# Kernel tuning notes

Measured on AMD Instinct MI355X. Metric: run time of the kernel, lower is better.

The kernel has to match this reference:

```python
import jax, jax.numpy as jnp
import numpy as np


def _l2norm(t, eps=1e-12):
    # matches torch F.normalize(p=2, dim=-1): x / max(||x||_2, eps)
    n = jnp.sqrt(jnp.sum(t * t, axis=-1, keepdims=True))
    return t / jnp.maximum(n, eps)


def setup_inputs() -> dict:
    key = jax.random.key(0)
    ks = jax.random.split(key, 8)
    B, N, C, H, W = 16, 4, 256, 64, 64
    d = 64  # dim_head
    x = jax.random.normal(ks[0], (B, C, H, W), jnp.float32)
    fmaps = jax.random.normal(ks[1], (B, N, C, H, W), jnp.float32)
    Wq = jax.random.normal(ks[2], (N * d, C), jnp.float32) * 0.02   # Linear [out,in]
    Wk = jax.random.normal(ks[3], (N, d, C), jnp.float32) * 0.02    # grouped 1x1 conv, per-group [d,C]
    Wv = jax.random.normal(ks[4], (N, d, C), jnp.float32) * 0.02
    rescale = jnp.ones((N, 1, 1), jnp.float32)
    Wffn = jax.random.normal(ks[5], (C, N * d), jnp.float32) * 0.02
    bffn = jnp.zeros((C,), jnp.float32)
    return {"x": x, "fmaps": fmaps, "Wq": Wq, "Wk": Wk, "Wv": Wv,
            "rescale": rescale, "Wffn": Wffn, "bffn": bffn}


def reference(x, fmaps, Wq, Wk, Wv, rescale, Wffn, bffn):
    B, N, C, H, W = fmaps.shape
    d = Wk.shape[1]
    HW = H * W

    # x: [B,C,H,W] -> tokens [B,HW,C]
    x_in = jnp.transpose(x, (0, 2, 3, 1)).reshape(B, HW, C)
    q_in = jnp.einsum('bsc,oc->bso', x_in, Wq)            # [B,HW,N*d]

    # grouped 1x1 convs on fmaps (group = fmap index n)
    fm = fmaps.reshape(B, N, C, HW)                       # [B,N,C,HW]
    k = jnp.einsum('bncs,ndc->bnds', fm, Wk)              # [B,N,d,HW]
    v = jnp.einsum('bncs,ndc->bnds', fm, Wv)              # [B,N,d,HW]

    q = jnp.transpose(q_in.reshape(B, HW, N, d), (0, 2, 3, 1))  # [B,N,d,HW]

    qn = _l2norm(q)   # normalize over spatial (HW) axis
    kn = _l2norm(k)

    attn = jnp.einsum('bnds,bnes->bnde', kn, qn) * rescale      # [B,N,d,d]
    attn = jax.nn.softmax(attn, axis=-1)
    out = jnp.einsum('bnde,bnes->bnds', attn, v)                # [B,N,d,HW]

    out = jnp.transpose(out, (0, 3, 1, 2)).reshape(B, HW, N * d)  # [B,HW,N*d]
    out = out + q_in
    out = jnp.einsum('bsi,ci->bsc', out, Wffn) + bffn + q_in      # ffn + residual
    return jnp.transpose(out.reshape(B, H, W, C), (0, 3, 1, 2))   # [B,C,H,W]
```

## Files before the change

kernel.cpp:

```cpp
#include <hip/hip_runtime.h>
#include <hip/hip_bf16.h>
#include <cmath>

using bf16 = __hip_bfloat16;
typedef __attribute__((ext_vector_type(4))) float  f32x4;
typedef __attribute__((ext_vector_type(8))) short  bf16x8;
typedef unsigned int u32;
typedef unsigned short u16;

__device__ __forceinline__ void gl_lds16(const bf16* g, bf16* l) {
    __builtin_amdgcn_global_load_lds(
        (const __attribute__((address_space(1))) u32*)g,
        (__attribute__((address_space(3))) u32*)l, 16, 0, 0);
}

__device__ __forceinline__ u32 pk2(float a, float b) {
    bf16 ha = __float2bfloat16(a), hb = __float2bfloat16(b);
    return (u32)*(u16*)&ha | ((u32)*(u16*)&hb << 16);
}
__device__ __forceinline__ float b2f(u16 v) {
    return __uint_as_float((u32)v << 16);
}

__global__ __launch_bounds__(256) void qproj(
    const float* __restrict__ x,
    const bf16* __restrict__ Wq,
    bf16* __restrict__ qch)
{
    __shared__ bf16 sW[128 * 64];
    __shared__ bf16 sX[128 * 72];
    const int t = threadIdx.x;
    const int lane = t & 63, wid = t >> 6;
    const int wm = wid >> 1, wn = wid & 1;
    const int g = lane >> 4, lr = lane & 15;
    const int s0 = blockIdx.x * 128;
    const int o0 = blockIdx.y * 128;
    const float* xb = x + (long)blockIdx.z * 1048576;

    f32x4 acc[4][4];
#pragma unroll
    for (int i = 0; i < 4; ++i)
#pragma unroll
        for (int j = 0; j < 4; ++j) acc[i][j] = (f32x4){0.f, 0.f, 0.f, 0.f};

    const int p  = t & 31;
    const int sl = t >> 5;

    for (int c0 = 0; c0 < 256; c0 += 64) {
        __syncthreads();
#pragma unroll
        for (int i = 0; i < 4; ++i) {
            int lin = i * 256 + t, r = lin >> 3, ch = lin & 7;
            gl_lds16(Wq + (long)(o0 + r) * 256 + c0 + ((ch ^ (r & 7)) << 3), &sW[lin * 8]);
        }
#pragma unroll
        for (int j = 0; j < 4; ++j) {
            int s4 = j * 8 + sl;
            const float* src = xb + (long)(c0 + 2 * p) * 4096 + s0 + s4 * 4;
            float4 a = *(const float4*)src;
            float4 bq = *(const float4*)(src + 4096);
            char* base = (char*)sX + p * 4 + (s4 * 4) * 144;
            *(u32*)(base +   0) = pk2(a.x, bq.x);
            *(u32*)(base + 144) = pk2(a.y, bq.y);
            *(u32*)(base + 288) = pk2(a.z, bq.z);
            *(u32*)(base + 432) = pk2(a.w, bq.w);
        }
        __syncthreads();
#pragma unroll
        for (int kk = 0; kk < 2; ++kk) {
            bf16x8 aw[4], fx[4];
#pragma unroll
            for (int mf = 0; mf < 4; ++mf) {
                int r = wm * 64 + mf * 16 + lr;
                int ch = (kk * 4 + g) ^ (r & 7);
                aw[mf] = *(const bf16x8*)((const char*)sW + r * 128 + ch * 16);
            }
#pragma unroll
            for (int nf = 0; nf < 4; ++nf) {
                int s = wn * 64 + nf * 16 + lr;
                fx[nf] = *(const bf16x8*)((const char*)sX + s * 144 + (kk * 4 + g) * 16);
            }
#pragma unroll
            for (int mf = 0; mf < 4; ++mf)
#pragma unroll
                for (int nf = 0; nf < 4; ++nf)
                    acc[mf][nf] = __builtin_amdgcn_mfma_f32_16x16x32_bf16(
                        aw[mf], fx[nf], acc[mf][nf], 0, 0, 0);
        }
    }
    bf16* qb = qch + (long)blockIdx.z * 1048576;
#pragma unroll
    for (int mf = 0; mf < 4; ++mf)
#pragma unroll
        for (int nf = 0; nf < 4; ++nf)
#pragma unroll
            for (int e = 0; e < 4; ++e) {
                int o = o0 + wm * 64 + mf * 16 + g * 4 + e;
                int s = s0 + wn * 64 + nf * 16 + lr;
                qb[(long)o * 4096 + s] = __float2bfloat16(acc[mf][nf][e]);
            }
}

__global__ __launch_bounds__(256) void kvproj(
    const float* __restrict__ fm,
    const bf16* __restrict__ Wk,
    const bf16* __restrict__ Wv,
    bf16* __restrict__ kb,
    bf16* __restrict__ vT)
{
    __shared__ bf16 sF[128 * 72];
    __shared__ bf16 sK[64 * 64];
    __shared__ bf16 sV[64 * 64];
    const int t = threadIdx.x;
    const int lane = t & 63, wid = t >> 6;
    const int g = lane >> 4, lr = lane & 15;
    const int s0 = blockIdx.x * 128;
    const int bn = blockIdx.y, n = bn & 3;
    const float* fb = fm + (long)bn * 1048576;
    const bf16* WkN = Wk + (long)n * 16384;
    const bf16* WvN = Wv + (long)n * 16384;

    f32x4 acc1[4][2];
    f32x4 acc2[2][4];
#pragma unroll
    for (int i = 0; i < 4; ++i)
#pragma unroll
        for (int j = 0; j < 2; ++j) {
            acc1[i][j] = (f32x4){0.f, 0.f, 0.f, 0.f};
            acc2[j][i] = (f32x4){0.f, 0.f, 0.f, 0.f};
        }

    const int p  = t & 31;
    const int sl = t >> 5;

    for (int c0 = 0; c0 < 256; c0 += 64) {
        __syncthreads();
#pragma unroll
        for (int i = 0; i < 2; ++i) {
            int lin = i * 256 + t, r = lin >> 3, ch = lin & 7;
            int srcoff = r * 256 + c0 + ((ch ^ (r & 7)) << 3);
            gl_lds16(WkN + srcoff, &sK[lin * 8]);
            gl_lds16(WvN + srcoff, &sV[lin * 8]);
        }
#pragma unroll
        for (int j = 0; j < 4; ++j) {
            int s4 = j * 8 + sl;
            const float* src = fb + (long)(c0 + 2 * p) * 4096 + s0 + s4 * 4;
            float4 a = *(const float4*)src;
            float4 bq = *(const float4*)(src + 4096);
            char* base = (char*)sF + p * 4 + (s4 * 4) * 144;
            *(u32*)(base +   0) = pk2(a.x, bq.x);
            *(u32*)(base + 144) = pk2(a.y, bq.y);
            *(u32*)(base + 288) = pk2(a.z, bq.z);
            *(u32*)(base + 432) = pk2(a.w, bq.w);
        }
        __syncthreads();
#pragma unroll
        for (int kk = 0; kk < 2; ++kk) {
            bf16x8 ak[4], ff[2], bv[4];
#pragma unroll
            for (int mf = 0; mf < 4; ++mf) {
                int r = mf * 16 + lr;
                int ch = (kk * 4 + g) ^ (r & 7);
                ak[mf] = *(const bf16x8*)((const char*)sK + r * 128 + ch * 16);
            }
#pragma unroll
            for (int i = 0; i < 2; ++i) {
                int s = wid * 32 + i * 16 + lr;
                ff[i] = *(const bf16x8*)((const char*)sF + s * 144 + (kk * 4 + g) * 16);
            }
#pragma unroll
            for (int nf = 0; nf < 4; ++nf) {
                int r = nf * 16 + lr;
                int ch = (kk * 4 + g) ^ (r & 7);
                bv[nf] = *(const bf16x8*)((const char*)sV + r * 128 + ch * 16);
            }
#pragma unroll
            for (int mf = 0; mf < 4; ++mf)
#pragma unroll
                for (int i = 0; i < 2; ++i)
                    acc1[mf][i] = __builtin_amdgcn_mfma_f32_16x16x32_bf16(
                        ak[mf], ff[i], acc1[mf][i], 0, 0, 0);
#pragma unroll
            for (int i = 0; i < 2; ++i)
#pragma unroll
                for (int nf = 0; nf < 4; ++nf)
                    acc2[i][nf] = __builtin_amdgcn_mfma_f32_16x16x32_bf16(
                        ff[i], bv[nf], acc2[i][nf], 0, 0, 0);
        }
    }
    bf16* kbb = kb + (long)bn * 262144;
#pragma unroll
    for (int mf = 0; mf < 4; ++mf)
#pragma unroll
        for (int i = 0; i < 2; ++i)
#pragma unroll
            for (int e = 0; e < 4; ++e) {
                int dd = mf * 16 + g * 4 + e;
                int s  = s0 + wid * 32 + i * 16 + lr;
                kbb[(long)dd * 4096 + s] = __float2bfloat16(acc1[mf][i][e]);
            }
    bf16* vtb = vT + (long)bn * 262144;
#pragma unroll
    for (int i = 0; i < 2; ++i)
#pragma unroll
        for (int nf = 0; nf < 4; ++nf)
#pragma unroll
            for (int e = 0; e < 4; ++e) {
                int s = s0 + wid * 32 + i * 16 + g * 4 + e;
                int ec = nf * 16 + lr;
                vtb[(long)s * 64 + ec] = __float2bfloat16(acc2[i][nf][e]);
            }
}

__global__ __launch_bounds__(256) void qk_sum(
    const bf16* __restrict__ kb,
    const bf16* __restrict__ qch,
    float* __restrict__ part,
    float* __restrict__ sumq, float* __restrict__ sumk)
{
    __shared__ bf16 sA[64 * 64];
    __shared__ bf16 sB[64 * 64];
    const int t = threadIdx.x;
    const int lane = t & 63, wid = t >> 6;
    const int wm = wid >> 1, wn = wid & 1;
    const int g = lane >> 4, lr = lane & 15;
    const int ch_ = blockIdx.x;
    const int bn = blockIdx.y;
    const bf16* kbase = kb + (long)bn * 262144;
    const bf16* qbase = qch + (long)bn * 262144;

    const int srow = t >> 1;
    const int shalf = t & 1;

    f32x4 acc[2][2];
#pragma unroll
    for (int i = 0; i < 2; ++i)
#pragma unroll
        for (int j = 0; j < 2; ++j) acc[i][j] = (f32x4){0.f, 0.f, 0.f, 0.f};
    float ss = 0.f;

    for (int it = 0; it < 16; ++it) {
        int k0 = ch_ * 1024 + it * 64;
        __syncthreads();
#pragma unroll
        for (int i = 0; i < 2; ++i) {
            int lin = i * 256 + t, r = lin >> 3, c = lin & 7;
            gl_lds16(kbase + (long)r * 4096 + k0 + ((c ^ (r & 7)) << 3), &sA[lin * 8]);
            gl_lds16(qbase + (long)r * 4096 + k0 + ((c ^ (r & 7)) << 3), &sB[lin * 8]);
        }
        __syncthreads();
#pragma unroll
        for (int kk = 0; kk < 2; ++kk) {
            bf16x8 af[2], bf[2];
#pragma unroll
            for (int mf = 0; mf < 2; ++mf) {
                int r = wm * 32 + mf * 16 + lr;
                af[mf] = *(const bf16x8*)((const char*)sA + r * 128 + (((kk * 4 + g) ^ (r & 7)) << 4));
            }
#pragma unroll
            for (int nf = 0; nf < 2; ++nf) {
                int r = wn * 32 + nf * 16 + lr;
                bf[nf] = *(const bf16x8*)((const char*)sB + r * 128 + (((kk * 4 + g) ^ (r & 7)) << 4));
            }
#pragma unroll
            for (int mf = 0; mf < 2; ++mf)
#pragma unroll
                for (int nf = 0; nf < 2; ++nf)
                    acc[mf][nf] = __builtin_amdgcn_mfma_f32_16x16x32_bf16(
                        af[mf], bf[nf], acc[mf][nf], 0, 0, 0);
        }
        {
            const char* base = (srow < 64) ? (const char*)sA + srow * 128
                                           : (const char*)sB + (srow - 64) * 128;
            int r7 = srow & 7;
#pragma unroll
            for (int j = 0; j < 4; ++j) {
                bf16x8 v = *(const bf16x8*)(base + (((shalf * 4 + j) ^ r7) << 4));
#pragma unroll
                for (int e = 0; e < 8; ++e) {
                    float f = b2f((u16)v[e]);
                    ss += f * f;
                }
            }
        }
    }
    ss += __shfl_xor(ss, 1);
    if (shalf == 0) {
        if (srow < 64) atomicAdd(&sumk[bn * 64 + srow], ss);
        else           atomicAdd(&sumq[bn * 64 + srow - 64], ss);
    }
    float* pp = part + ((long)bn * 4 + ch_) * 4096;
#pragma unroll
    for (int mf = 0; mf < 2; ++mf)
#pragma unroll
        for (int nf = 0; nf < 2; ++nf)
#pragma unroll
            for (int e = 0; e < 4; ++e) {
                int m = wm * 32 + mf * 16 + g * 4 + e;
                int nn = wn * 32 + nf * 16 + lr;
                pp[m * 64 + nn] = acc[mf][nf][e];
            }
}

__global__ __launch_bounds__(256) void attn_finalize_kernel(
    const float* __restrict__ part,
    const float* __restrict__ sumq, const float* __restrict__ sumk,
    const float* __restrict__ rescale,
    bf16* __restrict__ attn_out)
{
    const int bn = blockIdx.x;
    const int n = bn & 3;
    const int t = threadIdx.x;
    const float rs = rescale[n];

    __shared__ float att[64][65];
    __shared__ float rmax[64], rsum[64];
    __shared__ float iq[64], ik[64];

    if (t < 64)        ik[t]      = 1.f / fmaxf(sqrtf(sumk[bn * 64 + t]), 1e-12f);
    else if (t < 128)  iq[t - 64] = 1.f / fmaxf(sqrtf(sumq[bn * 64 + t - 64]), 1e-12f);
    __syncthreads();

    const float* pb = part + (size_t)bn * 4 * 4096;
#pragma unroll
    for (int p = 0; p < 16; ++p) {
        int lin = p * 256 + t;
        int dd = lin >> 6, e = lin & 63;
        float v = pb[lin] + pb[4096 + lin] + pb[8192 + lin] + pb[12288 + lin];
        v *= ik[dd] * iq[e] * rs;
        att[dd][e] = v;
    }
    __syncthreads();
    if (t < 64) {
        float m = -1e30f;
        for (int e = 0; e < 64; ++e) m = fmaxf(m, att[t][e]);
        float sm = 0.f;
        for (int e = 0; e < 64; ++e) sm += expf(att[t][e] - m);
        rmax[t] = m;
        rsum[t] = 1.0f / sm;
    }
    __syncthreads();
    bf16* ob = attn_out + (size_t)bn * 4096;
#pragma unroll
    for (int p = 0; p < 16; ++p) {
        int lin = p * 256 + t;
        int dd = lin >> 6, e = lin & 63;
        ob[lin] = __float2bfloat16(expf(att[dd][e] - rmax[dd]) * rsum[dd]);
    }
}

__global__ __launch_bounds__(256) void pvffn(
    const bf16* __restrict__ vT,
    const bf16* __restrict__ attnb,
    const bf16* __restrict__ qch,
    const bf16* __restrict__ Wf,
    const float* __restrict__ bffn,
    float* __restrict__ out)
{
    __shared__ bf16 bufX[256 * 64];
    __shared__ bf16 Zs[128 * 64];
    const int t = threadIdx.x;
    const int lane = t & 63, wid = t >> 6;
    const int g = lane >> 4, lr = lane & 15;
    const int s0 = blockIdx.x * 128;
    const int b = blockIdx.y;

    f32x4 accF[4][8];
#pragma unroll
    for (int i = 0; i < 4; ++i)
#pragma unroll
        for (int j = 0; j < 8; ++j) accF[i][j] = (f32x4){0.f, 0.f, 0.f, 0.f};

    for (int n = 0; n < 4; ++n) {
        const int bn = b * 4 + n;
        __syncthreads();
#pragma unroll
        for (int i = 0; i < 4; ++i) {
            int lin = i * 256 + t, r = lin >> 3, c = lin & 7;
            gl_lds16(vT + (long)bn * 262144 + (long)(s0 + r) * 64 + ((c ^ (r & 7)) << 3),
                     &bufX[lin * 8]);
        }
#pragma unroll
        for (int i = 0; i < 2; ++i) {
            int lin = i * 256 + t, r = lin >> 3, c = lin & 7;
            gl_lds16(attnb + (long)bn * 4096 + r * 64 + ((c ^ (r & 7)) << 3),
                     &bufX[8192 + lin * 8]);
        }
        __syncthreads();
        f32x4 accP[2][4];
#pragma unroll
        for (int i = 0; i < 2; ++i)
#pragma unroll
            for (int j = 0; j < 4; ++j) accP[i][j] = (f32x4){0.f, 0.f, 0.f, 0.f};
#pragma unroll
        for (int kk = 0; kk < 2; ++kk) {
            bf16x8 av[2], at[4];
#pragma unroll
            for (int mf = 0; mf < 2; ++mf) {
                int r = wid * 32 + mf * 16 + lr;
                av[mf] = *(const bf16x8*)((const char*)bufX + r * 128 + (((kk * 4 + g) ^ (r & 7)) << 4));
            }
#pragma unroll
            for (int nf = 0; nf < 4; ++nf) {
                int r = nf * 16 + lr;
                at[nf] = *(const bf16x8*)((const char*)bufX + 16384 + r * 128 + (((kk * 4 + g) ^ (r & 7)) << 4));
            }
#pragma unroll
            for (int mf = 0; mf < 2; ++mf)
#pragma unroll
                for (int nf = 0; nf < 4; ++nf)
                    accP[mf][nf] = __builtin_amdgcn_mfma_f32_16x16x32_bf16(
                        av[mf], at[nf], accP[mf][nf], 0, 0, 0);
        }
#pragma unroll
        for (int mf = 0; mf < 2; ++mf)
#pragma unroll
            for (int nf = 0; nf < 4; ++nf) {
                int slb = wid * 32 + mf * 16 + g * 4;
                int il = nf * 16 + lr;
                ushort4 qv = *(const ushort4*)(qch + ((long)b * 256 + n * 64 + il) * 4096 + s0 + slb);
                u16 qa[4] = {qv.x, qv.y, qv.z, qv.w};
#pragma unroll
                for (int e = 0; e < 4; ++e) {
                    int sl = slb + e;
                    float v = accP[mf][nf][e] + b2f(qa[e]);
                    bf16 hv = __float2bfloat16(v);
                    int byte = sl * 128 + ((((il >> 3) ^ (sl & 7))) << 4) + (il & 7) * 2;
                    *(u16*)((char*)Zs + byte) = *(u16*)&hv;
                }
            }
        __syncthreads();
#pragma unroll
        for (int i = 0; i < 8; ++i) {
            int lin = i * 256 + t, r = lin >> 3, c = lin & 7;
            gl_lds16(Wf + (long)r * 256 + n * 64 + ((c ^ (r & 7)) << 3), &bufX[lin * 8]);
        }
        __syncthreads();
#pragma unroll
        for (int kk = 0; kk < 2; ++kk) {
            bf16x8 aw[4], bz[8];
#pragma unroll
            for (int mf = 0; mf < 4; ++mf) {
                int r = wid * 64 + mf * 16 + lr;
                aw[mf] = *(const bf16x8*)((const char*)bufX + r * 128 + (((kk * 4 + g) ^ (r & 7)) << 4));
            }
#pragma unroll
            for (int nf = 0; nf < 8; ++nf) {
                int sl = nf * 16 + lr;
                bz[nf] = *(const bf16x8*)((const char*)Zs + sl * 128 + (((kk * 4 + g) ^ (sl & 7)) << 4));
            }
#pragma unroll
            for (int mf = 0; mf < 4; ++mf)
#pragma unroll
                for (int nf = 0; nf < 8; ++nf)
                    accF[mf][nf] = __builtin_amdgcn_mfma_f32_16x16x32_bf16(
                        aw[mf], bz[nf], accF[mf][nf], 0, 0, 0);
        }
    }
    float* ob = out + (long)b * 1048576;
    const bf16* qb = qch + (long)b * 1048576;
#pragma unroll
    for (int mf = 0; mf < 4; ++mf)
#pragma unroll
        for (int e = 0; e < 4; ++e) {
            int c = wid * 64 + mf * 16 + g * 4 + e;
            float bv = bffn[c];
#pragma unroll
            for (int nf = 0; nf < 8; ++nf) {
                int s = s0 + nf * 16 + lr;
                long idx = (long)c * 4096 + s;
                ob[idx] = accF[mf][nf][e] + bv + b2f(*(const u16*)(qb + idx));
            }
        }
}

__global__ __launch_bounds__(256) void wconv(
    const float* __restrict__ a, const float* __restrict__ b,
    const float* __restrict__ c, const float* __restrict__ d,
    bf16* __restrict__ o)
{
    int i = blockIdx.x * 256 + threadIdx.x;
    int which = i >> 16, off = i & 65535;
    const float* s = (which == 0) ? a : (which == 1) ? b : (which == 2) ? c : d;
    o[i] = __float2bfloat16(s[off]);
}

extern "C" void kernel_launch(void* const* d_in, const int* in_sizes, int n_in,
                              void* d_out, int out_size, void* d_ws, size_t ws_size,
                              hipStream_t stream) {
    const float* x       = (const float*)d_in[0];
    const float* fmaps   = (const float*)d_in[1];
    const float* Wq      = (const float*)d_in[2];
    const float* Wk      = (const float*)d_in[3];
    const float* Wv      = (const float*)d_in[4];
    const float* rescale = (const float*)d_in[5];
    const float* Wffn    = (const float*)d_in[6];
    const float* bffn    = (const float*)d_in[7];
    float* out = (float*)d_out;

    char* w = (char*)d_ws;
    bf16* kbuf  = (bf16*)(w + 0);
    bf16* vT    = (bf16*)(w + 33554432L);
    bf16* qch   = (bf16*)(w + 67108864L);
    float* part = (float*)(w + 100663296L);
    bf16* attnb = (bf16*)(w + 104857600L);
    float* sumq = (float*)(w + 105381888L);
    float* sumk = (float*)(w + 105398272L);
    bf16* Wq_b  = (bf16*)(w + 105414656L);
    bf16* Wk_b  = Wq_b + 65536;
    bf16* Wv_b  = Wq_b + 131072;
    bf16* Wf_b  = Wq_b + 196608;

    dim3 blk(256);

    hipMemsetAsync(sumq, 0, 32768, stream);
    wconv<<<dim3(1024), blk, 0, stream>>>(Wq, Wk, Wv, Wffn, Wq_b);
    kvproj<<<dim3(32, 64), blk, 0, stream>>>(fmaps, Wk_b, Wv_b, kbuf, vT);
    qproj<<<dim3(32, 2, 16), blk, 0, stream>>>(x, Wq_b, qch);
    qk_sum<<<dim3(4, 64), blk, 0, stream>>>(kbuf, qch, part, sumq, sumk);
    attn_finalize_kernel<<<dim3(64), blk, 0, stream>>>(part, sumq, sumk, rescale, attnb);
    pvffn<<<dim3(32, 16), blk, 0, stream>>>(vT, attnb, qch, Wf_b, bffn, out);
}
```

Before: 200.9 us.

## Fold attention into FFN weights and fuse K projection with QK reduction

Restructures the pipeline algebraically. Wffn·attn is precomputed per batch into M2, and Wffn·Wq + Wq into WQF, so the final output becomes one GEMM over [vT; x_bf16] with K=512. This removes the per-tile PV product and the Z staging in LDS. K projection is fused into the QK-sum kernel so the k buffer is never written to memory, and qproj also emits a bf16 copy of x. The exchange is extra weight-prep kernels, a longer K dimension in the output GEMM, and slightly different rounding from folding the weights in bf16.

```diff
diff --git a/kernel.cpp b/kernel.cpp
--- a/kernel.cpp
+++ b/kernel.cpp
@@ -13,466 +13,12 @@
         (const __attribute__((address_space(1))) u32*)g,
         (__attribute__((address_space(3))) u32*)l, 16, 0, 0);
 }
-
 __device__ __forceinline__ u32 pk2(float a, float b) {
     bf16 ha = __float2bfloat16(a), hb = __float2bfloat16(b);
     return (u32)*(u16*)&ha | ((u32)*(u16*)&hb << 16);
 }
 __device__ __forceinline__ float b2f(u16 v) {
     return __uint_as_float((u32)v << 16);
-}
-
-__global__ __launch_bounds__(256) void qproj(
-    const float* __restrict__ x,
-    const bf16* __restrict__ Wq,
-    bf16* __restrict__ qch)
-{
-    __shared__ bf16 sW[128 * 64];
-    __shared__ bf16 sX[128 * 72];
-    const int t = threadIdx.x;
-    const int lane = t & 63, wid = t >> 6;
-    const int wm = wid >> 1, wn = wid & 1;
-    const int g = lane >> 4, lr = lane & 15;
-    const int s0 = blockIdx.x * 128;
-    const int o0 = blockIdx.y * 128;
-    const float* xb = x + (long)blockIdx.z * 1048576;
-
-    f32x4 acc[4][4];
-#pragma unroll
-    for (int i = 0; i < 4; ++i)
-#pragma unroll
-        for (int j = 0; j < 4; ++j) acc[i][j] = (f32x4){0.f, 0.f, 0.f, 0.f};
-
-    const int p  = t & 31;
-    const int sl = t >> 5;
-
-    for (int c0 = 0; c0 < 256; c0 += 64) {
-        __syncthreads();
-#pragma unroll
-        for (int i = 0; i < 4; ++i) {
-            int lin = i * 256 + t, r = lin >> 3, ch = lin & 7;
-            gl_lds16(Wq + (long)(o0 + r) * 256 + c0 + ((ch ^ (r & 7)) << 3), &sW[lin * 8]);
-        }
-#pragma unroll
-        for (int j = 0; j < 4; ++j) {
-            int s4 = j * 8 + sl;
-            const float* src = xb + (long)(c0 + 2 * p) * 4096 + s0 + s4 * 4;
-            float4 a = *(const float4*)src;
-            float4 bq = *(const float4*)(src + 4096);
-            char* base = (char*)sX + p * 4 + (s4 * 4) * 144;
-            *(u32*)(base +   0) = pk2(a.x, bq.x);
-            *(u32*)(base + 144) = pk2(a.y, bq.y);
-            *(u32*)(base + 288) = pk2(a.z, bq.z);
-            *(u32*)(base + 432) = pk2(a.w, bq.w);
-        }
-        __syncthreads();
-#pragma unroll
-        for (int kk = 0; kk < 2; ++kk) {
-            bf16x8 aw[4], fx[4];
-#pragma unroll
-            for (int mf = 0; mf < 4; ++mf) {
-                int r = wm * 64 + mf * 16 + lr;
-                int ch = (kk * 4 + g) ^ (r & 7);
-                aw[mf] = *(const bf16x8*)((const char*)sW + r * 128 + ch * 16);
-            }
-#pragma unroll
-            for (int nf = 0; nf < 4; ++nf) {
-                int s = wn * 64 + nf * 16 + lr;
-                fx[nf] = *(const bf16x8*)((const char*)sX + s * 144 + (kk * 4 + g) * 16);
-            }
-#pragma unroll
-            for (int mf = 0; mf < 4; ++mf)
-#pragma unroll
-                for (int nf = 0; nf < 4; ++nf)
-                    acc[mf][nf] = __builtin_amdgcn_mfma_f32_16x16x32_bf16(
-                        aw[mf], fx[nf], acc[mf][nf], 0, 0, 0);
-        }
-    }
-    bf16* qb = qch + (long)blockIdx.z * 1048576;
-#pragma unroll
-    for (int mf = 0; mf < 4; ++mf)
-#pragma unroll
-        for (int nf = 0; nf < 4; ++nf)
-#pragma unroll
-            for (int e = 0; e < 4; ++e) {
-                int o = o0 + wm * 64 + mf * 16 + g * 4 + e;
-                int s = s0 + wn * 64 + nf * 16 + lr;
-                qb[(long)o * 4096 + s] = __float2bfloat16(acc[mf][nf][e]);
-            }
-}
-
-__global__ __launch_bounds__(256) void kvproj(
-    const float* __restrict__ fm,
-    const bf16* __restrict__ Wk,
-    const bf16* __restrict__ Wv,
-    bf16* __restrict__ kb,
-    bf16* __restrict__ vT)
-{
-    __shared__ bf16 sF[128 * 72];
-    __shared__ bf16 sK[64 * 64];
-    __shared__ bf16 sV[64 * 64];
-    const int t = threadIdx.x;
-    const int lane = t & 63, wid = t >> 6;
-    const int g = lane >> 4, lr = lane & 15;
-    const int s0 = blockIdx.x * 128;
-    const int bn = blockIdx.y, n = bn & 3;
-    const float* fb = fm + (long)bn * 1048576;
-    const bf16* WkN = Wk + (long)n * 16384;
-    const bf16* WvN = Wv + (long)n * 16384;
-
-    f32x4 acc1[4][2];
-    f32x4 acc2[2][4];
-#pragma unroll
-    for (int i = 0; i < 4; ++i)
-#pragma unroll
-        for (int j = 0; j < 2; ++j) {
-            acc1[i][j] = (f32x4){0.f, 0.f, 0.f, 0.f};
-            acc2[j][i] = (f32x4){0.f, 0.f, 0.f, 0.f};
-        }
-
-    const int p  = t & 31;
-    const int sl = t >> 5;
-
-    for (int c0 = 0; c0 < 256; c0 += 64) {
-        __syncthreads();
-#pragma unroll
-        for (int i = 0; i < 2; ++i) {
-            int lin = i * 256 + t, r = lin >> 3, ch = lin & 7;
-            int srcoff = r * 256 + c0 + ((ch ^ (r & 7)) << 3);
-            gl_lds16(WkN + srcoff, &sK[lin * 8]);
-            gl_lds16(WvN + srcoff, &sV[lin * 8]);
-        }
-#pragma unroll
-        for (int j = 0; j < 4; ++j) {
-            int s4 = j * 8 + sl;
-            const float* src = fb + (long)(c0 + 2 * p) * 4096 + s0 + s4 * 4;
-            float4 a = *(const float4*)src;
-            float4 bq = *(const float4*)(src + 4096);
-            char* base = (char*)sF + p * 4 + (s4 * 4) * 144;
-            *(u32*)(base +   0) = pk2(a.x, bq.x);
-            *(u32*)(base + 144) = pk2(a.y, bq.y);
-            *(u32*)(base + 288) = pk2(a.z, bq.z);
-            *(u32*)(base + 432) = pk2(a.w, bq.w);
-        }
-        __syncthreads();
-#pragma unroll
-        for (int kk = 0; kk < 2; ++kk) {
-            bf16x8 ak[4], ff[2], bv[4];
-#pragma unroll
-            for (int mf = 0; mf < 4; ++mf) {
-                int r = mf * 16 + lr;
-                int ch = (kk * 4 + g) ^ (r & 7);
-                ak[mf] = *(const bf16x8*)((const char*)sK + r * 128 + ch * 16);
-            }
-#pragma unroll
-            for (int i = 0; i < 2; ++i) {
-                int s = wid * 32 + i * 16 + lr;
-                ff[i] = *(const bf16x8*)((const char*)sF + s * 144 + (kk * 4 + g) * 16);
-            }
-#pragma unroll
-            for (int nf = 0; nf < 4; ++nf) {
-                int r = nf * 16 + lr;
-                int ch = (kk * 4 + g) ^ (r & 7);
-                bv[nf] = *(const bf16x8*)((const char*)sV + r * 128 + ch * 16);
-            }
-#pragma unroll
-            for (int mf = 0; mf < 4; ++mf)
-#pragma unroll
-                for (int i = 0; i < 2; ++i)
-                    acc1[mf][i] = __builtin_amdgcn_mfma_f32_16x16x32_bf16(
-                        ak[mf], ff[i], acc1[mf][i], 0, 0, 0);
-#pragma unroll
-            for (int i = 0; i < 2; ++i)
-#pragma unroll
-                for (int nf = 0; nf < 4; ++nf)
-                    acc2[i][nf] = __builtin_amdgcn_mfma_f32_16x16x32_bf16(
-                        ff[i], bv[nf], acc2[i][nf], 0, 0, 0);
-        }
-    }
-    bf16* kbb = kb + (long)bn * 262144;
-#pragma unroll
-    for (int mf = 0; mf < 4; ++mf)
-#pragma unroll
-        for (int i = 0; i < 2; ++i)
-#pragma unroll
-            for (int e = 0; e < 4; ++e) {
-                int dd = mf * 16 + g * 4 + e;
-                int s  = s0 + wid * 32 + i * 16 + lr;
-                kbb[(long)dd * 4096 + s] = __float2bfloat16(acc1[mf][i][e]);
-            }
-    bf16* vtb = vT + (long)bn * 262144;
-#pragma unroll
-    for (int i = 0; i < 2; ++i)
-#pragma unroll
-        for (int nf = 0; nf < 4; ++nf)
-#pragma unroll
-            for (int e = 0; e < 4; ++e) {
-                int s = s0 + wid * 32 + i * 16 + g * 4 + e;
-                int ec = nf * 16 + lr;
-                vtb[(long)s * 64 + ec] = __float2bfloat16(acc2[i][nf][e]);
-            }
-}
-
-__global__ __launch_bounds__(256) void qk_sum(
-    const bf16* __restrict__ kb,
-    const bf16* __restrict__ qch,
-    float* __restrict__ part,
-    float* __restrict__ sumq, float* __restrict__ sumk)
-{
-    __shared__ bf16 sA[64 * 64];
-    __shared__ bf16 sB[64 * 64];
-    const int t = threadIdx.x;
-    const int lane = t & 63, wid = t >> 6;
-    const int wm = wid >> 1, wn = wid & 1;
-    const int g = lane >> 4, lr = lane & 15;
-    const int ch_ = blockIdx.x;
-    const int bn = blockIdx.y;
-    const bf16* kbase = kb + (long)bn * 262144;
-    const bf16* qbase = qch + (long)bn * 262144;
-
-    const int srow = t >> 1;
-    const int shalf = t & 1;
-
-    f32x4 acc[2][2];
-#pragma unroll
-    for (int i = 0; i < 2; ++i)
-#pragma unroll
-        for (int j = 0; j < 2; ++j) acc[i][j] = (f32x4){0.f, 0.f, 0.f, 0.f};
-    float ss = 0.f;
-
-    for (int it = 0; it < 16; ++it) {
-        int k0 = ch_ * 1024 + it * 64;
-        __syncthreads();
-#pragma unroll
-        for (int i = 0; i < 2; ++i) {
-            int lin = i * 256 + t, r = lin >> 3, c = lin & 7;
-            gl_lds16(kbase + (long)r * 4096 + k0 + ((c ^ (r & 7)) << 3), &sA[lin * 8]);
-            gl_lds16(qbase + (long)r * 4096 + k0 + ((c ^ (r & 7)) << 3), &sB[lin * 8]);
-        }
-        __syncthreads();
-#pragma unroll
-        for (int kk = 0; kk < 2; ++kk) {
-            bf16x8 af[2], bf[2];
-#pragma unroll
-            for (int mf = 0; mf < 2; ++mf) {
-                int r = wm * 32 + mf * 16 + lr;
-                af[mf] = *(const bf16x8*)((const char*)sA + r * 128 + (((kk * 4 + g) ^ (r & 7)) << 4));
-            }
-#pragma unroll
-            for (int nf = 0; nf < 2; ++nf) {
-                int r = wn * 32 + nf * 16 + lr;
-                bf[nf] = *(const bf16x8*)((const char*)sB + r * 128 + (((kk * 4 + g) ^ (r & 7)) << 4));
-            }
-#pragma unroll
-            for (int mf = 0; mf < 2; ++mf)
-#pragma unroll
-                for (int nf = 0; nf < 2; ++nf)
-                    acc[mf][nf] = __builtin_amdgcn_mfma_f32_16x16x32_bf16(
-                        af[mf], bf[nf], acc[mf][nf], 0, 0, 0);
-        }
-        {
-            const char* base = (srow < 64) ? (const char*)sA + srow * 128
-                                           : (const char*)sB + (srow - 64) * 128;
-            int r7 = srow & 7;
-#pragma unroll
-            for (int j = 0; j < 4; ++j) {
-                bf16x8 v = *(const bf16x8*)(base + (((shalf * 4 + j) ^ r7) << 4));
-#pragma unroll
-                for (int e = 0; e < 8; ++e) {
-                    float f = b2f((u16)v[e]);
-                    ss += f * f;
-                }
-            }
-        }
-    }
-    ss += __shfl_xor(ss, 1);
-    if (shalf == 0) {
-        if (srow < 64) atomicAdd(&sumk[bn * 64 + srow], ss);
-        else           atomicAdd(&sumq[bn * 64 + srow - 64], ss);
-    }
-    float* pp = part + ((long)bn * 4 + ch_) * 4096;
-#pragma unroll
-    for (int mf = 0; mf < 2; ++mf)
-#pragma unroll
-        for (int nf = 0; nf < 2; ++nf)
-#pragma unroll
-            for (int e = 0; e < 4; ++e) {
-                int m = wm * 32 + mf * 16 + g * 4 + e;
-                int nn = wn * 32 + nf * 16 + lr;
-                pp[m * 64 + nn] = acc[mf][nf][e];
-            }
-}
-
-__global__ __launch_bounds__(256) void attn_finalize_kernel(
-    const float* __restrict__ part,
-    const float* __restrict__ sumq, const float* __restrict__ sumk,
-    const float* __restrict__ rescale,
-    bf16* __restrict__ attn_out)
-{
-    const int bn = blockIdx.x;
-    const int n = bn & 3;
-    const int t = threadIdx.x;
-    const float rs = rescale[n];
-
-    __shared__ float att[64][65];
-    __shared__ float rmax[64], rsum[64];
-    __shared__ float iq[64], ik[64];
-
-    if (t < 64)        ik[t]      = 1.f / fmaxf(sqrtf(sumk[bn * 64 + t]), 1e-12f);
-    else if (t < 128)  iq[t - 64] = 1.f / fmaxf(sqrtf(sumq[bn * 64 + t - 64]), 1e-12f);
-    __syncthreads();
-
-    const float* pb = part + (size_t)bn * 4 * 4096;
-#pragma unroll
-    for (int p = 0; p < 16; ++p) {
-        int lin = p * 256 + t;
-        int dd = lin >> 6, e = lin & 63;
-        float v = pb[lin] + pb[4096 + lin] + pb[8192 + lin] + pb[12288 + lin];
-        v *= ik[dd] * iq[e] * rs;
-        att[dd][e] = v;
-    }
-    __syncthreads();
-    if (t < 64) {
-        float m = -1e30f;
-        for (int e = 0; e < 64; ++e) m = fmaxf(m, att[t][e]);
-        float sm = 0.f;
-        for (int e = 0; e < 64; ++e) sm += expf(att[t][e] - m);
-        rmax[t] = m;
-        rsum[t] = 1.0f / sm;
-    }
-    __syncthreads();
-    bf16* ob = attn_out + (size_t)bn * 4096;
-#pragma unroll
-    for (int p = 0; p < 16; ++p) {
-        int lin = p * 256 + t;
-        int dd = lin >> 6, e = lin & 63;
-        ob[lin] = __float2bfloat16(expf(att[dd][e] - rmax[dd]) * rsum[dd]);
-    }
-}
-
-__global__ __launch_bounds__(256) void pvffn(
-    const bf16* __restrict__ vT,
-    const bf16* __restrict__ attnb,
-    const bf16* __restrict__ qch,
-    const bf16* __restrict__ Wf,
-    const float* __restrict__ bffn,
-    float* __restrict__ out)
-{
-    __shared__ bf16 bufX[256 * 64];
-    __shared__ bf16 Zs[128 * 64];
-    const int t = threadIdx.x;
-    const int lane = t & 63, wid = t >> 6;
-    const int g = lane >> 4, lr = lane & 15;
-    const int s0 = blockIdx.x * 128;
-    const int b = blockIdx.y;
-
-    f32x4 accF[4][8];
-#pragma unroll
-    for (int i = 0; i < 4; ++i)
-#pragma unroll
-        for (int j = 0; j < 8; ++j) accF[i][j] = (f32x4){0.f, 0.f, 0.f, 0.f};
-
-    for (int n = 0; n < 4; ++n) {
-        const int bn = b * 4 + n;
-        __syncthreads();
-#pragma unroll
-        for (int i = 0; i < 4; ++i) {
-            int lin = i * 256 + t, r = lin >> 3, c = lin & 7;
-            gl_lds16(vT + (long)bn * 262144 + (long)(s0 + r) * 64 + ((c ^ (r & 7)) << 3),
-                     &bufX[lin * 8]);
-        }
-#pragma unroll
-        for (int i = 0; i < 2; ++i) {
-            int lin = i * 256 + t, r = lin >> 3, c = lin & 7;
-            gl_lds16(attnb + (long)bn * 4096 + r * 64 + ((c ^ (r & 7)) << 3),
-                     &bufX[8192 + lin * 8]);
-        }
-        __syncthreads();
-        f32x4 accP[2][4];
-#pragma unroll
-        for (int i = 0; i < 2; ++i)
-#pragma unroll
-            for (int j = 0; j < 4; ++j) accP[i][j] = (f32x4){0.f, 0.f, 0.f, 0.f};
-#pragma unroll
-        for (int kk = 0; kk < 2; ++kk) {
-            bf16x8 av[2], at[4];
-#pragma unroll
-            for (int mf = 0; mf < 2; ++mf) {
-                int r = wid * 32 + mf * 16 + lr;
-                av[mf] = *(const bf16x8*)((const char*)bufX + r * 128 + (((kk * 4 + g) ^ (r & 7)) << 4));
-            }
-#pragma unroll
-            for (int nf = 0; nf < 4; ++nf) {
-                int r = nf * 16 + lr;
-                at[nf] = *(const bf16x8*)((const char*)bufX + 16384 + r * 128 + (((kk * 4 + g) ^ (r & 7)) << 4));
-            }
-#pragma unroll
-            for (int mf = 0; mf < 2; ++mf)
-#pragma unroll
-                for (int nf = 0; nf < 4; ++nf)
-                    accP[mf][nf] = __builtin_amdgcn_mfma_f32_16x16x32_bf16(
-                        av[mf], at[nf], accP[mf][nf], 0, 0, 0);
-        }
-#pragma unroll
-        for (int mf = 0; mf < 2; ++mf)
-#pragma unroll
-            for (int nf = 0; nf < 4; ++nf) {
-                int slb = wid * 32 + mf * 16 + g * 4;
-                int il = nf * 16 + lr;
-                ushort4 qv = *(const ushort4*)(qch + ((long)b * 256 + n * 64 + il) * 4096 + s0 + slb);
-                u16 qa[4] = {qv.x, qv.y, qv.z, qv.w};
-#pragma unroll
-                for (int e = 0; e < 4; ++e) {
-                    int sl = slb + e;
-                    float v = accP[mf][nf][e] + b2f(qa[e]);
-                    bf16 hv = __float2bfloat16(v);
-                    int byte = sl * 128 + ((((il >> 3) ^ (sl & 7))) << 4) + (il & 7) * 2;
-                    *(u16*)((char*)Zs + byte) = *(u16*)&hv;
-                }
-            }
-        __syncthreads();
-#pragma unroll
-        for (int i = 0; i < 8; ++i) {
-            int lin = i * 256 + t, r = lin >> 3, c = lin & 7;
-            gl_lds16(Wf + (long)r * 256 + n * 64 + ((c ^ (r & 7)) << 3), &bufX[lin * 8]);
-        }
-        __syncthreads();
-#pragma unroll
-        for (int kk = 0; kk < 2; ++kk) {
-            bf16x8 aw[4], bz[8];
-#pragma unroll
-            for (int mf = 0; mf < 4; ++mf) {
-                int r = wid * 64 + mf * 16 + lr;
-                aw[mf] = *(const bf16x8*)((const char*)bufX + r * 128 + (((kk * 4 + g) ^ (r & 7)) << 4));
-            }
-#pragma unroll
-            for (int nf = 0; nf < 8; ++nf) {
-                int sl = nf * 16 + lr;
-                bz[nf] = *(const bf16x8*)((const char*)Zs + sl * 128 + (((kk * 4 + g) ^ (sl & 7)) << 4));
-            }
-#pragma unroll
-            for (int mf = 0; mf < 4; ++mf)
-#pragma unroll
-                for (int nf = 0; nf < 8; ++nf)
-                    accF[mf][nf] = __builtin_amdgcn_mfma_f32_16x16x32_bf16(
-                        aw[mf], bz[nf], accF[mf][nf], 0, 0, 0);
-        }
-    }
-    float* ob = out + (long)b * 1048576;
-    const bf16* qb = qch + (long)b * 1048576;
-#pragma unroll
-    for (int mf = 0; mf < 4; ++mf)
-#pragma unroll
-        for (int e = 0; e < 4; ++e) {
-            int c = wid * 64 + mf * 16 + g * 4 + e;
-            float bv = bffn[c];
-#pragma unroll
-            for (int nf = 0; nf < 8; ++nf) {
-                int s = s0 + nf * 16 + lr;
-                long idx = (long)c * 4096 + s;
-                ob[idx] = accF[mf][nf][e] + bv + b2f(*(const u16*)(qb + idx));
-            }
-        }
 }
 
 __global__ __launch_bounds__(256) void wconv(
@@ -484,6 +30,451 @@
     int which = i >> 16, off = i & 65535;
     const float* s = (which == 0) ? a : (which == 1) ? b : (which == 2) ? c : d;
     o[i] = __float2bfloat16(s[off]);
+}
+
+__global__ __launch_bounds__(256) void wqf_kernel(
+    const float* __restrict__ Wffn, const float* __restrict__ Wq,
+    bf16* __restrict__ WQF)
+{
+    const int c = blockIdx.x, cp = threadIdx.x;
+    float acc = Wq[c * 256 + cp];
+#pragma unroll 8
+    for (int i = 0; i < 256; ++i)
+        acc += Wffn[c * 256 + i] * Wq[i * 256 + cp];
+    WQF[c * 256 + cp] = __float2bfloat16(acc);
+}
+
+__global__ __launch_bounds__(512) void qproj8(
+    const float* __restrict__ x,
+    const bf16* __restrict__ Wq,
+    bf16* __restrict__ qch,
+    bf16* __restrict__ xbf)
+{
+    __shared__ bf16 sW[256 * 64];
+    __shared__ bf16 sX[128 * 72];
+    const int t = threadIdx.x;
+    const int lane = t & 63, wid = t >> 6;
+    const int wm = wid >> 1, wn = wid & 1;
+    const int g = lane >> 4, lr = lane & 15;
+    const int s0 = blockIdx.x * 128;
+    const int b = blockIdx.y;
+    const float* xb = x + (long)b * 1048576;
+    bf16* xob = xbf + (long)b * 1048576;
+
+    f32x4 acc[4][4];
+#pragma unroll
+    for (int i = 0; i < 4; ++i)
+#pragma unroll
+        for (int j = 0; j < 4; ++j) acc[i][j] = (f32x4){0.f, 0.f, 0.f, 0.f};
+
+    const int p  = t & 31;
+    const int sl = t >> 5;
+
+    for (int c0 = 0; c0 < 256; c0 += 64) {
+        __syncthreads();
+#pragma unroll
+        for (int i = 0; i < 4; ++i) {
+            int lin = i * 512 + t, r = lin >> 3, ch = lin & 7;
+            gl_lds16(Wq + (long)r * 256 + c0 + ((ch ^ (r & 7)) << 3), &sW[lin * 8]);
+        }
+#pragma unroll
+        for (int j = 0; j < 2; ++j) {
+            int s4 = j * 16 + sl;
+            const float* src = xb + (long)(c0 + 2 * p) * 4096 + s0 + s4 * 4;
+            float4 a = *(const float4*)src;
+            float4 bq = *(const float4*)(src + 4096);
+            u32 w0 = pk2(a.x, bq.x), w1 = pk2(a.y, bq.y);
+            u32 w2 = pk2(a.z, bq.z), w3 = pk2(a.w, bq.w);
+            char* base = (char*)sX + p * 4 + (s4 * 4) * 144;
+            *(u32*)(base +   0) = w0;
+            *(u32*)(base + 144) = w1;
+            *(u32*)(base + 288) = w2;
+            *(u32*)(base + 432) = w3;
+            long xo = (long)(s0 + s4 * 4) * 256 + c0 + 2 * p;
+            *(u32*)(xob + xo)       = w0;
+            *(u32*)(xob + xo + 256) = w1;
+            *(u32*)(xob + xo + 512) = w2;
+            *(u32*)(xob + xo + 768) = w3;
+        }
+        __syncthreads();
+#pragma unroll
+        for (int kk = 0; kk < 2; ++kk) {
+            bf16x8 aw[4], fx[4];
+#pragma unroll
+            for (int mf = 0; mf < 4; ++mf) {
+                int r = wm * 64 + mf * 16 + lr;
+                aw[mf] = *(const bf16x8*)((const char*)sW + r * 128 + (((kk * 4 + g) ^ (r & 7)) << 4));
+            }
+#pragma unroll
+            for (int nf = 0; nf < 4; ++nf) {
+                int s = wn * 64 + nf * 16 + lr;
+                fx[nf] = *(const bf16x8*)((const char*)sX + s * 144 + (kk * 4 + g) * 16);
+            }
+#pragma unroll
+            for (int mf = 0; mf < 4; ++mf)
+#pragma unroll
+                for (int nf = 0; nf < 4; ++nf)
+                    acc[mf][nf] = __builtin_amdgcn_mfma_f32_16x16x32_bf16(
+                        aw[mf], fx[nf], acc[mf][nf], 0, 0, 0);
+        }
+    }
+    bf16* qb = qch + (long)b * 1048576;
+#pragma unroll
+    for (int mf = 0; mf < 4; ++mf)
+#pragma unroll
+        for (int nf = 0; nf < 4; ++nf)
+#pragma unroll
+            for (int e = 0; e < 4; ++e) {
+                int o = wm * 64 + mf * 16 + g * 4 + e;
+                int s = s0 + wn * 64 + nf * 16 + lr;
+                qb[(long)o * 4096 + s] = __float2bfloat16(acc[mf][nf][e]);
+            }
+}
+
+__global__ __launch_bounds__(256) void kvqk(
+    const float* __restrict__ fm,
+    const bf16* __restrict__ Wk,
+    const bf16* __restrict__ Wv,
+    const bf16* __restrict__ qch,
+    bf16* __restrict__ vT,
+    float* __restrict__ part,
+    float* __restrict__ sums)
+{
+    __shared__ bf16 sF[128 * 72];
+    __shared__ bf16 sWk[64 * 64];
+    __shared__ bf16 sWv[64 * 64];
+    __shared__ bf16 sKt[64 * 128];
+    __shared__ bf16 sQ[64 * 128];
+    const int t = threadIdx.x;
+    const int lane = t & 63, wid = t >> 6;
+    const int g = lane >> 4, lr = lane & 15;
+    const int ch_ = blockIdx.x;
+    const int bn = blockIdx.y, n = bn & 3;
+    const float* fb = fm + (long)bn * 1048576;
+    const bf16* WkN = Wk + (long)n * 16384;
+    const bf16* WvN = Wv + (long)n * 16384;
+    const bf16* qbase = qch + (long)bn * 262144;
+    bf16* vtb = vT + (long)bn * 262144;
+
+    const int p  = t & 31;
+    const int sl = t >> 5;
+    const int srow = t >> 1, shalf = t & 1;
+
+    f32x4 accQ[4];
+#pragma unroll
+    for (int i = 0; i < 4; ++i) accQ[i] = (f32x4){0.f, 0.f, 0.f, 0.f};
+    float ssum = 0.f;
+
+    for (int sub = 0; sub < 4; ++sub) {
+        const int ss0 = ch_ * 512 + sub * 128;
+        f32x4 acc1[4][2], acc2[2][4];
+#pragma unroll
+        for (int i = 0; i < 4; ++i)
+#pragma unroll
+            for (int j = 0; j < 2; ++j) {
+                acc1[i][j] = (f32x4){0.f, 0.f, 0.f, 0.f};
+                acc2[j][i] = (f32x4){0.f, 0.f, 0.f, 0.f};
+            }
+
+        for (int c0 = 0; c0 < 256; c0 += 64) {
+            __syncthreads();
+#pragma unroll
+            for (int i = 0; i < 2; ++i) {
+                int lin = i * 256 + t, r = lin >> 3, c = lin & 7;
+                int off = r * 256 + c0 + ((c ^ (r & 7)) << 3);
+                gl_lds16(WkN + off, &sWk[lin * 8]);
+                gl_lds16(WvN + off, &sWv[lin * 8]);
+            }
+#pragma unroll
+            for (int j = 0; j < 4; ++j) {
+                int s4 = j * 8 + sl;
+                const float* src = fb + (long)(c0 + 2 * p) * 4096 + ss0 + s4 * 4;
+                float4 a = *(const float4*)src;
+                float4 bq = *(const float4*)(src + 4096);
+                char* base = (char*)sF + p * 4 + (s4 * 4) * 144;
+                *(u32*)(base +   0) = pk2(a.x, bq.x);
+                *(u32*)(base + 144) = pk2(a.y, bq.y);
+                *(u32*)(base + 288) = pk2(a.z, bq.z);
+                *(u32*)(base + 432) = pk2(a.w, bq.w);
+            }
+            __syncthreads();
+#pragma unroll
+            for (int kk = 0; kk < 2; ++kk) {
+                bf16x8 ak[4], ff[2], bv[4];
+#pragma unroll
+                for (int mf = 0; mf < 4; ++mf) {
+                    int r = mf * 16 + lr;
+                    ak[mf] = *(const bf16x8*)((const char*)sWk + r * 128 + (((kk * 4 + g) ^ (r & 7)) << 4));
+                }
+#pragma unroll
+                for (int i = 0; i < 2; ++i) {
+                    int s = wid * 32 + i * 16 + lr;
+                    ff[i] = *(const bf16x8*)((const char*)sF + s * 144 + (kk * 4 + g) * 16);
+                }
+#pragma unroll
+                for (int nf = 0; nf < 4; ++nf) {
+                    int r = nf * 16 + lr;
+                    bv[nf] = *(const bf16x8*)((const char*)sWv + r * 128 + (((kk * 4 + g) ^ (r & 7)) << 4));
+                }
+#pragma unroll
+                for (int mf = 0; mf < 4; ++mf)
+#pragma unroll
+                    for (int i = 0; i < 2; ++i)
+                        acc1[mf][i] = __builtin_amdgcn_mfma_f32_16x16x32_bf16(
+                            ak[mf], ff[i], acc1[mf][i], 0, 0, 0);
+#pragma unroll
+                for (int i = 0; i < 2; ++i)
+#pragma unroll
+                    for (int nf = 0; nf < 4; ++nf)
+                        acc2[i][nf] = __builtin_amdgcn_mfma_f32_16x16x32_bf16(
+                            ff[i], bv[nf], acc2[i][nf], 0, 0, 0);
+            }
+        }
+#pragma unroll
+        for (int i = 0; i < 4; ++i) {
+            int lin = i * 256 + t, r = lin >> 4, c = lin & 15;
+            gl_lds16(qbase + (long)r * 4096 + ss0 + ((c ^ (r & 7)) << 3), &sQ[lin * 8]);
+        }
+#pragma unroll
+        for (int i = 0; i < 2; ++i)
+#pragma unroll
+            for (int nf = 0; nf < 4; ++nf)
+#pragma unroll
+                for (int e = 0; e < 4; ++e) {
+                    int s = ss0 + wid * 32 + i * 16 + g * 4 + e;
+                    vtb[(long)s * 64 + nf * 16 + lr] = __float2bfloat16(acc2[i][nf][e]);
+                }
+#pragma unroll
+        for (int mf = 0; mf < 4; ++mf)
+#pragma unroll
+            for (int i = 0; i < 2; ++i)
+#pragma unroll
+                for (int e = 0; e < 4; ++e) {
+                    int dd = mf * 16 + g * 4 + e;
+                    int sc = wid * 32 + i * 16 + lr;
+                    bf16 hv = __float2bfloat16(acc1[mf][i][e]);
+                    int byte = (dd * 256 + sc * 2) ^ ((dd & 7) << 4);
+                    *(u16*)((char*)sKt + byte) = *(u16*)&hv;
+                }
+        __syncthreads();
+#pragma unroll
+        for (int kks = 0; kks < 4; ++kks) {
+            int rA = wid * 16 + lr;
+            bf16x8 af = *(const bf16x8*)((const char*)sKt + rA * 256 + (((kks * 4 + g) ^ (rA & 7)) << 4));
+            bf16x8 bq[4];
+#pragma unroll
+            for (int nf = 0; nf < 4; ++nf) {
+                int rB = nf * 16 + lr;
+                bq[nf] = *(const bf16x8*)((const char*)sQ + rB * 256 + (((kks * 4 + g) ^ (rB & 7)) << 4));
+            }
+#pragma unroll
+            for (int nf = 0; nf < 4; ++nf)
+                accQ[nf] = __builtin_amdgcn_mfma_f32_16x16x32_bf16(
+                    af, bq[nf], accQ[nf], 0, 0, 0);
+        }
+        {
+            const char* base = (srow < 64) ? (const char*)sKt + srow * 256
+                                           : (const char*)sQ + (srow - 64) * 256;
+            int r7 = srow & 7;
+#pragma unroll
+            for (int j = 0; j < 8; ++j) {
+                bf16x8 v = *(const bf16x8*)(base + (((shalf * 8 + j) ^ r7) << 4));
+#pragma unroll
+                for (int e = 0; e < 8; ++e) {
+                    float f = b2f((u16)v[e]);
+                    ssum += f * f;
+                }
+            }
+        }
+    }
+    float* pp = part + ((long)bn * 8 + ch_) * 4096;
+#pragma unroll
+    for (int nf = 0; nf < 4; ++nf)
+#pragma unroll
+        for (int e = 0; e < 4; ++e) {
+            int dd = wid * 16 + g * 4 + e;
+            pp[dd * 64 + nf * 16 + lr] = accQ[nf][e];
+        }
+    ssum += __shfl_xor(ssum, 1);
+    if (shalf == 0) {
+        if (srow < 64) atomicAdd(&sums[4096 + bn * 64 + srow], ssum);
+        else           atomicAdd(&sums[bn * 64 + (srow - 64)], ssum);
+    }
+}
+
+__global__ __launch_bounds__(256) void finalizeM2(
+    const float* __restrict__ part, const float* __restrict__ sums,
+    const float* __restrict__ rescale, const bf16* __restrict__ Wf,
+    bf16* __restrict__ M2)
+{
+    __shared__ float att[64][65];
+    __shared__ float rmax[64], rsm[64], iq[64], ik[64];
+    __shared__ bf16 sWf[256 * 64];
+    __shared__ bf16 attT[64 * 64];
+    const int bn = blockIdx.x, n = bn & 3, b = bn >> 2;
+    const int t = threadIdx.x;
+    const int lane = t & 63, wid = t >> 6;
+    const int g = lane >> 4, lr = lane & 15;
+    const float rs = rescale[n];
+
+#pragma unroll
+    for (int i = 0; i < 8; ++i) {
+        int lin = i * 256 + t, r = lin >> 3, c = lin & 7;
+        gl_lds16(Wf + (long)r * 256 + n * 64 + ((c ^ (r & 7)) << 3), &sWf[lin * 8]);
+    }
+    if (t < 64)        ik[t]      = 1.f / fmaxf(sqrtf(sums[4096 + bn * 64 + t]), 1e-12f);
+    else if (t < 128)  iq[t - 64] = 1.f / fmaxf(sqrtf(sums[bn * 64 + t - 64]), 1e-12f);
+    __syncthreads();
+
+    const float* pb = part + (long)bn * 8 * 4096;
+#pragma unroll
+    for (int p_ = 0; p_ < 16; ++p_) {
+        int lin = p_ * 256 + t;
+        int dd = lin >> 6, e = lin & 63;
+        float v = 0.f;
+#pragma unroll
+        for (int c = 0; c < 8; ++c) v += pb[c * 4096 + lin];
+        att[dd][e] = v * ik[dd] * iq[e] * rs;
+    }
+    __syncthreads();
+    if (t < 64) {
+        float m = -1e30f;
+        for (int e = 0; e < 64; ++e) m = fmaxf(m, att[t][e]);
+        float sm = 0.f;
+        for (int e = 0; e < 64; ++e) sm += expf(att[t][e] - m);
+        rmax[t] = m;
+        rsm[t] = 1.0f / sm;
+    }
+    __syncthreads();
+#pragma unroll
+    for (int p_ = 0; p_ < 16; ++p_) {
+        int lin = p_ * 256 + t;
+        int dd = lin >> 6, e = lin & 63;
+        bf16 hv = __float2bfloat16(expf(att[dd][e] - rmax[dd]) * rsm[dd]);
+        int byte = (e * 128 + dd * 2) ^ ((e & 7) << 4);
+        *(u16*)((char*)attT + byte) = *(u16*)&hv;
+    }
+    __syncthreads();
+
+    f32x4 acc[4][4];
+#pragma unroll
+    for (int i = 0; i < 4; ++i)
+#pragma unroll
+        for (int j = 0; j < 4; ++j) acc[i][j] = (f32x4){0.f, 0.f, 0.f, 0.f};
+#pragma unroll
+    for (int kk = 0; kk < 2; ++kk) {
+        bf16x8 aw[4], bt[4];
+#pragma unroll
+        for (int mf = 0; mf < 4; ++mf) {
+            int r = wid * 64 + mf * 16 + lr;
+            aw[mf] = *(const bf16x8*)((const char*)sWf + r * 128 + (((kk * 4 + g) ^ (r & 7)) << 4));
+        }
+#pragma unroll
+        for (int nf = 0; nf < 4; ++nf) {
+            int e = nf * 16 + lr;
+            bt[nf] = *(const bf16x8*)((const char*)attT + e * 128 + (((kk * 4 + g) ^ (e & 7)) << 4));
+        }
+#pragma unroll
+        for (int mf = 0; mf < 4; ++mf)
+#pragma unroll
+            for (int nf = 0; nf < 4; ++nf)
+                acc[mf][nf] = __builtin_amdgcn_mfma_f32_16x16x32_bf16(
+                    aw[mf], bt[nf], acc[mf][nf], 0, 0, 0);
+    }
+    bf16* m2b = M2 + (long)b * 65536;
+#pragma unroll
+    for (int mf = 0; mf < 4; ++mf)
+#pragma unroll
+        for (int nf = 0; nf < 4; ++nf)
+#pragma unroll
+            for (int e = 0; e < 4; ++e) {
+                int c = wid * 64 + mf * 16 + g * 4 + e;
+                m2b[c * 256 + n * 64 + nf * 16 + lr] = __float2bfloat16(acc[mf][nf][e]);
+            }
+}
+
+__global__ __launch_bounds__(512) void outgemm(
+    const bf16* __restrict__ M2,
+    const bf16* __restrict__ WQF,
+    const bf16* __restrict__ vT,
+    const bf16* __restrict__ xbf,
+    const float* __restrict__ bffn,
+    float* __restrict__ out)
+{
+    __shared__ bf16 sA[256 * 64];
+    __shared__ bf16 sB[128 * 64];
+    const int t = threadIdx.x;
+    const int lane = t & 63, wid = t >> 6;
+    const int wm = wid >> 1, wn = wid & 1;
+    const int g = lane >> 4, lr = lane & 15;
+    const int s0 = blockIdx.x * 128;
+    const int b = blockIdx.y;
+
+    f32x4 acc[4][4];
+#pragma unroll
+    for (int i = 0; i < 4; ++i)
+#pragma unroll
+        for (int j = 0; j < 4; ++j) acc[i][j] = (f32x4){0.f, 0.f, 0.f, 0.f};
+
+    for (int ch = 0; ch < 8; ++ch) {
+        const bf16* Asrc;
+        const bf16* Bsrc;
+        int Brs;
+        if (ch < 4) {
+            Asrc = M2 + (long)b * 65536 + ch * 64;
+            Bsrc = vT + ((long)b * 4 + ch) * 262144 + (long)s0 * 64;
+            Brs = 64;
+        } else {
+            Asrc = WQF + (ch - 4) * 64;
+            Bsrc = xbf + (long)b * 1048576 + (long)s0 * 256 + (ch - 4) * 64;
+            Brs = 256;
+        }
+        __syncthreads();
+#pragma unroll
+        for (int i = 0; i < 4; ++i) {
+            int lin = i * 512 + t, r = lin >> 3, c = lin & 7;
+            gl_lds16(Asrc + (long)r * 256 + ((c ^ (r & 7)) << 3), &sA[lin * 8]);
+        }
+#pragma unroll
+        for (int i = 0; i < 2; ++i) {
+            int lin = i * 512 + t, r = lin >> 3, c = lin & 7;
+            gl_lds16(Bsrc + (long)r * Brs + ((c ^ (r & 7)) << 3), &sB[lin * 8]);
+        }
+        __syncthreads();
+#pragma unroll
+        for (int kk = 0; kk < 2; ++kk) {
+            bf16x8 aw[4], bz[4];
+#pragma unroll
+            for (int mf = 0; mf < 4; ++mf) {
+                int r = wm * 64 + mf * 16 + lr;
+                aw[mf] = *(const bf16x8*)((const char*)sA + r * 128 + (((kk * 4 + g) ^ (r & 7)) << 4));
+            }
+#pragma unroll
+            for (int nf = 0; nf < 4; ++nf) {
+                int r = wn * 64 + nf * 16 + lr;
+                bz[nf] = *(const bf16x8*)((const char*)sB + r * 128 + (((kk * 4 + g) ^ (r & 7)) << 4));
+            }
+#pragma unroll
+            for (int mf = 0; mf < 4; ++mf)
+#pragma unroll
+                for (int nf = 0; nf < 4; ++nf)
+                    acc[mf][nf] = __builtin_amdgcn_mfma_f32_16x16x32_bf16(
+                        aw[mf], bz[nf], acc[mf][nf], 0, 0, 0);
+        }
+    }
+    float* ob = out + (long)b * 1048576;
+#pragma unroll
+    for (int mf = 0; mf < 4; ++mf)
+#pragma unroll
+        for (int e = 0; e < 4; ++e) {
+            int c = wm * 64 + mf * 16 + g * 4 + e;
+            float bv = bffn[c];
+#pragma unroll
+            for (int nf = 0; nf < 4; ++nf) {
+                int s = s0 + wn * 64 + nf * 16 + lr;
+                ob[(long)c * 4096 + s] = acc[mf][nf][e] + bv;
+            }
+        }
 }
 
 extern "C" void kernel_launch(void* const* d_in, const int* in_sizes, int n_in,
@@ -500,25 +491,25 @@
     float* out = (float*)d_out;
 
     char* w = (char*)d_ws;
-    bf16* kbuf  = (bf16*)(w + 0);
+    bf16* qch   = (bf16*)(w + 0);
     bf16* vT    = (bf16*)(w + 33554432L);
-    bf16* qch   = (bf16*)(w + 67108864L);
+    bf16* xbf   = (bf16*)(w + 67108864L);
     float* part = (float*)(w + 100663296L);
-    bf16* attnb = (bf16*)(w + 104857600L);
-    float* sumq = (float*)(w + 105381888L);
-    float* sumk = (float*)(w + 105398272L);
-    bf16* Wq_b  = (bf16*)(w + 105414656L);
+    float* sums = (float*)(w + 109051904L);
+    bf16* M2    = (bf16*)(w + 109084672L);
+    bf16* Wq_b  = (bf16*)(w + 111181824L);
     bf16* Wk_b  = Wq_b + 65536;
     bf16* Wv_b  = Wq_b + 131072;
     bf16* Wf_b  = Wq_b + 196608;
+    bf16* WQF   = (bf16*)(w + 111706112L);
 
     dim3 blk(256);
 
-    hipMemsetAsync(sumq, 0, 32768, stream);
+    hipMemsetAsync(sums, 0, 32768, stream);
     wconv<<<dim3(1024), blk, 0, stream>>>(Wq, Wk, Wv, Wffn, Wq_b);
-    kvproj<<<dim3(32, 64), blk, 0, stream>>>(fmaps, Wk_b, Wv_b, kbuf, vT);
-    qproj<<<dim3(32, 2, 16), blk, 0, stream>>>(x, Wq_b, qch);
-    qk_sum<<<dim3(4, 64), blk, 0, stream>>>(kbuf, qch, part, sumq, sumk);
-    attn_finalize_kernel<<<dim3(64), blk, 0, stream>>>(part, sumq, sumk, rescale, attnb);
-    pvffn<<<dim3(32, 16), blk, 0, stream>>>(vT, attnb, qch, Wf_b, bffn, out);
-}
+    wqf_kernel<<<dim3(256), blk, 0, stream>>>(Wffn, Wq, WQF);
+    qproj8<<<dim3(32, 16), dim3(512), 0, stream>>>(x, Wq_b, qch, xbf);
+    kvqk<<<dim3(8, 64), blk, 0, stream>>>(fmaps, Wk_b, Wv_b, qch, vT, part, sums);
+    finalizeM2<<<dim3(64), blk, 0, stream>>>(part, sums, rescale, Wf_b, M2);
+    outgemm<<<dim3(32, 16), dim3(512), 0, stream>>>(M2, WQF, vT, xbf, bffn, out);
+}
```

Result: slower. 209.2 us (+4.1%).
